# Kernel tuning notes

Measured on AMD Instinct MI355X. Metric: run time of the kernel, lower is better.

The kernel has to match this reference:

```python
import jax, jax.numpy as jnp
import numpy as np

NUM_CLASSES = 96
FEAT_DIM = 1024
BATCH = 65536


def setup_inputs() -> dict:
    key = jax.random.key(0)
    k1, k2, k3 = jax.random.split(key, 3)
    features = jax.random.normal(k1, (BATCH, FEAT_DIM), dtype=jnp.float32)
    labels = jax.random.randint(k2, (BATCH,), 0, NUM_CLASSES, dtype=jnp.int64)
    centers = jax.random.normal(k3, (NUM_CLASSES, FEAT_DIM), dtype=jnp.float32)
    return {"features": features, "centers": centers, "labels": labels}


def reference(features, centers, labels):
    batch_size = features.shape[0]
    num_classes = centers.shape[0]
    centers = centers.astype(features.dtype)
    # squared L2 distances: ||f||^2 + ||c||^2 - 2 f.c  -> [B, C]
    features_sq = jnp.sum(features * features, axis=1, keepdims=True)  # [B,1]
    centers_sq = jnp.sum(centers * centers, axis=1)                    # [C]
    distmat = features_sq + centers_sq[None, :] - 2.0 * jnp.einsum('bd,cd->bc', features, centers)
    # keep only the true-label column (mask applied BEFORE clamp, as in torch)
    mask = (labels[:, None] == jnp.arange(num_classes)[None, :]).astype(distmat.dtype)
    dist = distmat * mask
    loss = jnp.clip(dist, 1e-12, 1e12).sum() / batch_size
    return loss
```

## Files before the change

### kernel.cpp

```cpp
#include <hip/hip_runtime.h>

#define BATCH 65536
#define FEAT 1024
#define NCLS 96
#define NBLOCKS 1024
#define NTHREADS 256

__global__ __launch_bounds__(NTHREADS) void center_loss_partial(
    const float* __restrict__ features,
    const float* __restrict__ centers,
    const int* __restrict__ labels,
    float* __restrict__ partials)
{
    const int lane = threadIdx.x & 63;
    const int waveInBlock = threadIdx.x >> 6;
    const int wavesPerBlock = NTHREADS >> 6;
    const int globalWave = blockIdx.x * wavesPerBlock + waveInBlock;
    const int totalWaves = NBLOCKS * wavesPerBlock;

    float acc = 0.f;
    for (int row = globalWave; row < BATCH; row += totalWaves) {
        const int lbl = labels[row];
        const float4* f4 = (const float4*)(features + (size_t)row * FEAT);
        const float4* c4 = (const float4*)(centers + (size_t)lbl * FEAT);
        float fsq = 0.f, csq = 0.f, dot = 0.f;
#pragma unroll
        for (int it = 0; it < FEAT / 256; ++it) {
            const float4 f = f4[it * 64 + lane];
            const float4 c = c4[it * 64 + lane];
            fsq += f.x * f.x + f.y * f.y + f.z * f.z + f.w * f.w;
            csq += c.x * c.x + c.y * c.y + c.z * c.z + c.w * c.w;
            dot += f.x * c.x + f.y * c.y + f.z * c.z + f.w * c.w;
        }
#pragma unroll
        for (int off = 32; off > 0; off >>= 1) {
            fsq += __shfl_xor(fsq, off, 64);
            csq += __shfl_xor(csq, off, 64);
            dot += __shfl_xor(dot, off, 64);
        }
        float d = fsq + csq - 2.0f * dot;
        d = fminf(fmaxf(d, 1e-12f), 1e12f);
        acc += d;
    }

    __shared__ float wave_sums[NTHREADS / 64];
    if (lane == 0) wave_sums[waveInBlock] = acc;
    __syncthreads();
    if (threadIdx.x == 0) {
        float s = 0.f;
        for (int w = 0; w < wavesPerBlock; ++w) s += wave_sums[w];
        partials[blockIdx.x] = s;
    }
}

__global__ __launch_bounds__(256) void center_loss_final(
    const float* __restrict__ partials, float* __restrict__ out)
{
    __shared__ double sh[256];
    double s = 0.0;
    for (int i = threadIdx.x; i < NBLOCKS; i += 256) s += (double)partials[i];
    sh[threadIdx.x] = s;
    __syncthreads();
    for (int stride = 128; stride > 0; stride >>= 1) {
        if (threadIdx.x < stride) sh[threadIdx.x] += sh[threadIdx.x + stride];
        __syncthreads();
    }
    if (threadIdx.x == 0) {
        const double masked = (double)(NCLS - 1) * 1e-12;
        out[0] = (float)(sh[0] / (double)BATCH + masked);
    }
}

extern "C" void kernel_launch(void* const* d_in, const int* in_sizes, int n_in,
                              void* d_out, int out_size, void* d_ws, size_t ws_size,
                              hipStream_t stream) {
    const float* features = (const float*)d_in[0];
    const float* centers  = (const float*)d_in[1];
    const int*   labels   = (const int*)d_in[2];
    float* out = (float*)d_out;
    float* partials = (float*)d_ws;

    center_loss_partial<<<NBLOCKS, NTHREADS, 0, stream>>>(features, centers, labels, partials);
    center_loss_final<<<1, 256, 0, stream>>>(partials, out);
}
```

Measured before the change: 356.8 us.

## Flatten to elementwise grid-stride loop using squared difference per row

Replaces the per-row wave reduction with a flat grid-stride loop over all float4 elements. Each thread accumulates (f-c)^2 directly, and the per-row clamp is dropped. The shuffle reduction now runs once per thread at the end instead of once per row, and the block count is doubled. The row clamp is skipped, which holds because squared distances are nonnegative and the upper bound is unlikely to be reached, though it does differ from the reference when d would be below 1e-12. The change also computes the distance with a different formula, which alters rounding.

```diff
diff --git a/kernel.cpp b/kernel.cpp
--- a/kernel.cpp
+++ b/kernel.cpp
@@ -3,52 +3,43 @@
 #define BATCH 65536
 #define FEAT 1024
 #define NCLS 96
-#define NBLOCKS 1024
-#define NTHREADS 256
+#define NB 2048
+#define NT 256
+#define NV (BATCH * (FEAT / 4))
 
-__global__ __launch_bounds__(NTHREADS) void center_loss_partial(
+__global__ __launch_bounds__(NT) void center_loss_elem(
     const float* __restrict__ features,
     const float* __restrict__ centers,
     const int* __restrict__ labels,
     float* __restrict__ partials)
 {
-    const int lane = threadIdx.x & 63;
-    const int waveInBlock = threadIdx.x >> 6;
-    const int wavesPerBlock = NTHREADS >> 6;
-    const int globalWave = blockIdx.x * wavesPerBlock + waveInBlock;
-    const int totalWaves = NBLOCKS * wavesPerBlock;
+    const int tid = blockIdx.x * NT + threadIdx.x;
+    const int stride = NB * NT;
+    const float4* __restrict__ f4 = (const float4*)features;
+    const float4* __restrict__ c4 = (const float4*)centers;
 
     float acc = 0.f;
-    for (int row = globalWave; row < BATCH; row += totalWaves) {
+    for (int i = tid; i < NV; i += stride) {
+        const int row = i >> 8;
+        const int k4  = i & 255;
         const int lbl = labels[row];
-        const float4* f4 = (const float4*)(features + (size_t)row * FEAT);
-        const float4* c4 = (const float4*)(centers + (size_t)lbl * FEAT);
-        float fsq = 0.f, csq = 0.f, dot = 0.f;
-#pragma unroll
-        for (int it = 0; it < FEAT / 256; ++it) {
-            const float4 f = f4[it * 64 + lane];
-            const float4 c = c4[it * 64 + lane];
-            fsq += f.x * f.x + f.y * f.y + f.z * f.z + f.w * f.w;
-            csq += c.x * c.x + c.y * c.y + c.z * c.z + c.w * c.w;
-            dot += f.x * c.x + f.y * c.y + f.z * c.z + f.w * c.w;
-        }
-#pragma unroll
-        for (int off = 32; off > 0; off >>= 1) {
-            fsq += __shfl_xor(fsq, off, 64);
-            csq += __shfl_xor(csq, off, 64);
-            dot += __shfl_xor(dot, off, 64);
-        }
-        float d = fsq + csq - 2.0f * dot;
-        d = fminf(fmaxf(d, 1e-12f), 1e12f);
-        acc += d;
+        const float4 f = f4[i];
+        const float4 c = c4[(size_t)lbl * (FEAT / 4) + k4];
+        const float dx = f.x - c.x, dy = f.y - c.y;
+        const float dz = f.z - c.z, dw = f.w - c.w;
+        acc += dx * dx + dy * dy + dz * dz + dw * dw;
     }
 
-    __shared__ float wave_sums[NTHREADS / 64];
-    if (lane == 0) wave_sums[waveInBlock] = acc;
+#pragma unroll
+    for (int off = 32; off > 0; off >>= 1) acc += __shfl_xor(acc, off, 64);
+
+    __shared__ float wave_sums[NT / 64];
+    if ((threadIdx.x & 63) == 0) wave_sums[threadIdx.x >> 6] = acc;
     __syncthreads();
     if (threadIdx.x == 0) {
         float s = 0.f;
-        for (int w = 0; w < wavesPerBlock; ++w) s += wave_sums[w];
+#pragma unroll
+        for (int w = 0; w < NT / 64; ++w) s += wave_sums[w];
         partials[blockIdx.x] = s;
     }
 }
@@ -58,7 +49,7 @@
 {
     __shared__ double sh[256];
     double s = 0.0;
-    for (int i = threadIdx.x; i < NBLOCKS; i += 256) s += (double)partials[i];
+    for (int i = threadIdx.x; i < NB; i += 256) s += (double)partials[i];
     sh[threadIdx.x] = s;
     __syncthreads();
     for (int stride = 128; stride > 0; stride >>= 1) {
@@ -80,6 +71,6 @@
     float* out = (float*)d_out;
     float* partials = (float*)d_ws;
 
-    center_loss_partial<<<NBLOCKS, NTHREADS, 0, stream>>>(features, centers, labels, partials);
+    center_loss_elem<<<NB, NT, 0, stream>>>(features, centers, labels, partials);
     center_loss_final<<<1, 256, 0, stream>>>(partials, out);
 }
```

Result: no change. 354.9 us (-0.5%).
